# Kernel optimization log

Hardware: AMD Instinct MI355X
Metric: run time of the kernel (lower is better)

Reference implementation:

```python
import jax, jax.numpy as jnp
import numpy as np

N, E, D, DE, DH = 8000, 15000, 128, 16, 128
NUM_STEPS = 3


def setup_inputs() -> dict:
    key = jax.random.key(0)
    ks = jax.random.split(key, 10)
    s = lambda k, shape, scale: jax.random.normal(k, shape, jnp.float32) * scale
    return {
        "x": jax.random.normal(ks[0], (N, D), jnp.float32),
        "edge_attr": jax.random.normal(ks[1], (E, DE), jnp.float32),
        "W0": s(ks[2], (D, D), 0.08),   # lin0
        "b0": jnp.zeros((D,), jnp.float32),
        "W1": s(ks[3], (DE, DH), 0.2),  # edge net layer 1
        "b1": jnp.zeros((DH,), jnp.float32),
        "W2": s(ks[4], (DH, D * D), 0.02),  # edge net layer 2 -> D*D
        "b2": jnp.zeros((D * D,), jnp.float32),
        "root": s(ks[5], (D, D), 0.08),  # NNConv root weight
        "bias": jnp.zeros((D,), jnp.float32),  # NNConv bias
        "Wm": s(ks[6], (2 * D, D), 0.08),  # message_layer
        "bm": jnp.zeros((D,), jnp.float32),
        "edge_index": jax.random.randint(ks[7], (2, E), 0, N, jnp.int32),
    }


def reference(x, edge_attr, W0, b0, W1, b1, W2, b2, root, bias, Wm, bm, edge_index):
    n, d = x.shape
    src, dst = edge_index[0], edge_index[1]  # source_to_target flow (PyG default)
    # edge-conditioned weight matrices, identical across steps since edge_attr is fixed: [E, D, D]
    ew = (jax.nn.relu(edge_attr @ W1 + b1) @ W2 + b2).reshape(-1, d, d)
    init = x
    out = jax.nn.relu(x @ W0 + b0)
    for _ in range(NUM_STEPS):
        # gather source features, per-edge matvec, scatter-add to destinations
        msg = jnp.einsum('ed,edo->eo', out[src], ew)  # [E, D]
        agg = jax.ops.segment_sum(msg, dst, num_segments=n)  # [N, D]
        m = jax.nn.relu(agg + out @ root + bias)  # NNConv with root_weight + bias, then relu
        out = jnp.concatenate([m, out], axis=1) @ Wm + bm  # message_layer
    return out + init
```

## Files before the change

kernel.cpp:

```cpp
#include <hip/hip_runtime.h>

#define NE   15000
#define NVX  8000
#define EPAD 15040
#define NT_E 235

typedef __attribute__((ext_vector_type(8))) short short8;
typedef __attribute__((ext_vector_type(4))) float f32x4;

static __device__ __forceinline__ unsigned short f2b(float f){
  unsigned int u = __float_as_uint(f);
  u += 0x7fffu + ((u >> 16) & 1u);
  return (unsigned short)(u >> 16);
}

__global__ __launch_bounds__(256) void k_cvt(const float* __restrict__ in,
                                             unsigned short* __restrict__ out, int n){
  int i = (blockIdx.x * 256 + threadIdx.x) * 4;
  if (i >= n) return;
  float4 v = *(const float4*)(in + i);
  ushort4 o;
  o.x = f2b(v.x); o.y = f2b(v.y); o.z = f2b(v.z); o.w = f2b(v.w);
  *(ushort4*)(out + i) = o;
}

__global__ __launch_bounds__(256) void k_h1(const float* __restrict__ ea,
                                            const float* __restrict__ W1,
                                            const float* __restrict__ b1,
                                            float* __restrict__ h1T){
  __shared__ float sW1[16*128];
  __shared__ float sb1[128];
  int t = threadIdx.x;
  #pragma unroll
  for (int i = 0; i < 8; ++i) sW1[i*256 + t] = W1[i*256 + t];
  if (t < 128) sb1[t] = b1[t];
  __syncthreads();
  int e = blockIdx.x * 64 + (t & 63);
  int hg = t >> 6;
  bool valid = e < NE;
  int esafe = valid ? e : 0;
  float a[16];
  #pragma unroll
  for (int i = 0; i < 4; ++i){
    float4 v = *(const float4*)(ea + (size_t)esafe*16 + i*4);
    a[i*4+0]=v.x; a[i*4+1]=v.y; a[i*4+2]=v.z; a[i*4+3]=v.w;
  }
  for (int hh = 0; hh < 32; ++hh){
    int h = hg*32 + hh;
    float s = sb1[h];
    #pragma unroll
    for (int k = 0; k < 16; ++k) s = fmaf(a[k], sW1[k*128 + h], s);
    s = fmaxf(s, 0.f);
    h1T[(size_t)h*EPAD + e] = valid ? s : 0.f;
  }
}

__global__ __launch_bounds__(256) void k_wt(const float* __restrict__ W2,
                                            const float* __restrict__ b2,
                                            const float* __restrict__ W0,
                                            const float* __restrict__ root,
                                            const float* __restrict__ Wm,
                                            unsigned short* __restrict__ W2T,
                                            unsigned short* __restrict__ sWt){
  int b = blockIdx.x;
  const float* src;
  unsigned short* out;
  if (b < 128)      { src = W2 + (size_t)b*16384; out = W2T + (size_t)b*16384; }
  else if (b == 128){ src = b2;                   out = W2T + (size_t)128*16384; }
  else {
    int s = b - 129;
    out = sWt + (size_t)s*16384;
    src = (s==0) ? W0 : (s==1) ? root : (s==2) ? Wm : (Wm + 128*128);
  }
  int t = threadIdx.x;
  int o = t & 127, half = t >> 7;
  for (int it = 0; it < 8; ++it){
    int d0 = half*64 + it*8;
    unsigned int pk[4];
    #pragma unroll
    for (int j = 0; j < 4; ++j){
      float v0 = src[(size_t)(d0 + 2*j    )*128 + o];
      float v1 = src[(size_t)(d0 + 2*j + 1)*128 + o];
      pk[j] = (unsigned int)f2b(v0) | ((unsigned int)f2b(v1) << 16);
    }
    unsigned int off = (unsigned int)(o*256 + d0*2) ^ (((unsigned int)(o & 7)) << 4);
    *(uint4*)((char*)out + off) = make_uint4(pk[0], pk[1], pk[2], pk[3]);
  }
}

__global__ __launch_bounds__(256,2) void k_big(const unsigned short* __restrict__ outcur,
                                               const unsigned short* __restrict__ W2T,
                                               const float* __restrict__ h1T,
                                               const int* __restrict__ eidx,
                                               float* __restrict__ agg){
  __shared__ __align__(16) unsigned short sX[64*128];
  __shared__ __align__(16) float          sH[64*64];
  __shared__ __align__(16) unsigned short sW[128*128];
  int t = threadIdx.x, l = t & 63, w = t >> 6;
  int tile = blockIdx.x >> 1, par = blockIdx.x & 1;
  int e0 = tile * 64;
  {
    int r = t >> 2, q = t & 3;
    int e = e0 + r;
    int srow = eidx[e < NE ? e : NE-1];
    const uint4* gp = (const uint4*)((const char*)outcur + (size_t)srow*256 + q*64);
    uint4* lp = (uint4*)((char*)sX + r*256 + q*64);
    #pragma unroll
    for (int i = 0; i < 4; ++i) lp[i] = gp[i];
  }
  {
    int hh = t >> 2, q = t & 3;
    int h = par + hh*2;
    const uint4* gp = (const uint4*)((const char*)h1T + ((size_t)h*EPAD + e0)*4 + q*64);
    uint4* lp = (uint4*)((char*)sH + hh*256 + q*64);
    #pragma unroll
    for (int i = 0; i < 4; ++i) lp[i] = gp[i];
  }
  __syncthreads();
  short8 af[4][4];
  #pragma unroll
  for (int mf = 0; mf < 4; ++mf)
    #pragma unroll
    for (int kf = 0; kf < 4; ++kf)
      af[mf][kf] = *(const short8*)((const char*)sX + (mf*16 + (l & 15))*256 + kf*64 + ((l >> 4)*16));
  f32x4 acc[4][2];
  #pragma unroll
  for (int mf = 0; mf < 4; ++mf)
    #pragma unroll
    for (int nf = 0; nf < 2; ++nf)
      acc[mf][nf] = (f32x4){0.f,0.f,0.f,0.f};
  const f32x4 zf = (f32x4){0.f,0.f,0.f,0.f};
  int nh = (par == 0) ? 65 : 64;
  for (int hh = 0; hh < nh; ++hh){
    int h = (hh < 64) ? (par + hh*2) : 128;
    __syncthreads();
    {
      const uint4* gp = (const uint4*)((const char*)W2T + (size_t)h*32768);
      uint4* lp = (uint4*)sW;
      #pragma unroll
      for (int i = 0; i < 8; ++i) lp[i*256 + t] = gp[i*256 + t];
    }
    __syncthreads();
    f32x4 hv[4];
    if (hh < 64){
      #pragma unroll
      for (int mf = 0; mf < 4; ++mf)
        hv[mf] = *(const f32x4*)((const char*)sH + hh*256 + mf*64 + ((l >> 4)*16));
    } else {
      #pragma unroll
      for (int mf = 0; mf < 4; ++mf){
        int rb = e0 + mf*16 + ((l >> 4) << 2);
        #pragma unroll
        for (int j = 0; j < 4; ++j) hv[mf][j] = (rb + j < NE) ? 1.f : 0.f;
      }
    }
    #pragma unroll
    for (int nf = 0; nf < 2; ++nf){
      int col = w*32 + nf*16 + (l & 15);
      unsigned int swz = ((unsigned int)(col & 7)) << 4;
      f32x4 Y[4];
      #pragma unroll
      for (int kf = 0; kf < 4; ++kf){
        short8 bfr = *(const short8*)((const char*)sW +
                        (((unsigned int)(col*256 + kf*64 + ((l >> 4)*16))) ^ swz));
        #pragma unroll
        for (int mf = 0; mf < 4; ++mf)
          Y[mf] = __builtin_amdgcn_mfma_f32_16x16x32_bf16(af[mf][kf], bfr,
                    (kf == 0) ? zf : Y[mf], 0, 0, 0);
      }
      #pragma unroll
      for (int mf = 0; mf < 4; ++mf)
        #pragma unroll
        for (int j = 0; j < 4; ++j)
          acc[mf][nf][j] = fmaf(hv[mf][j], Y[mf][j], acc[mf][nf][j]);
    }
  }
  #pragma unroll
  for (int mf = 0; mf < 4; ++mf){
    #pragma unroll
    for (int j = 0; j < 4; ++j){
      int e = e0 + mf*16 + ((l >> 4) << 2) + j;
      int dst = (e < NE) ? eidx[NE + e] : 0;
      float* ap = agg + (size_t)dst*128;
      #pragma unroll
      for (int nf = 0; nf < 2; ++nf){
        int col = w*32 + nf*16 + (l & 15);
        atomicAdd(ap + col, acc[mf][nf][j]);
      }
    }
  }
}

__global__ __launch_bounds__(256,2) void k_gsm(const unsigned short* __restrict__ Aa,
                                               const unsigned short* __restrict__ Wa,
                                               const unsigned short* __restrict__ Ab,
                                               const unsigned short* __restrict__ Wb,
                                               const float* __restrict__ addin,
                                               const float* __restrict__ bias,
                                               int do_relu,
                                               unsigned short* __restrict__ outb,
                                               float* __restrict__ outf){
  __shared__ __align__(16) unsigned short sA[64*128];
  __shared__ __align__(16) unsigned short sW[128*128];
  int t = threadIdx.x, l = t & 63, w = t >> 6;
  int r0 = blockIdx.x * 64;
  f32x4 acc[4][2];
  #pragma unroll
  for (int mf = 0; mf < 4; ++mf)
    #pragma unroll
    for (int nf = 0; nf < 2; ++nf)
      acc[mf][nf] = (f32x4){0.f,0.f,0.f,0.f};
  const unsigned short* A = Aa;
  const unsigned short* W = Wa;
  for (int pass = 0; pass < 2; ++pass){
    if (pass == 1){
      if (Ab == nullptr) break;
      A = Ab; W = Wb;
      __syncthreads();
    }
    {
      const uint4* gp = (const uint4*)((const char*)A + (size_t)r0*256);
      uint4* lp = (uint4*)sA;
      #pragma unroll
      for (int i = 0; i < 4; ++i) lp[i*256 + t] = gp[i*256 + t];
      const uint4* gw = (const uint4*)W;
      uint4* lw = (uint4*)sW;
      #pragma unroll
      for (int i = 0; i < 8; ++i) lw[i*256 + t] = gw[i*256 + t];
    }
    __syncthreads();
    short8 af[4][4];
    #pragma unroll
    for (int mf = 0; mf < 4; ++mf)
      #pragma unroll
      for (int kf = 0; kf < 4; ++kf)
        af[mf][kf] = *(const short8*)((const char*)sA + (mf*16 + (l & 15))*256 + kf*64 + ((l >> 4)*16));
    #pragma unroll
    for (int nf = 0; nf < 2; ++nf){
      int col = w*32 + nf*16 + (l & 15);
      unsigned int swz = ((unsigned int)(col & 7)) << 4;
      #pragma unroll
      for (int kf = 0; kf < 4; ++kf){
        short8 bfr = *(const short8*)((const char*)sW +
                        (((unsigned int)(col*256 + kf*64 + ((l >> 4)*16))) ^ swz));
        #pragma unroll
        for (int mf = 0; mf < 4; ++mf)
          acc[mf][nf] = __builtin_amdgcn_mfma_f32_16x16x32_bf16(af[mf][kf], bfr, acc[mf][nf], 0, 0, 0);
      }
    }
  }
  #pragma unroll
  for (int mf = 0; mf < 4; ++mf){
    #pragma unroll
    for (int nf = 0; nf < 2; ++nf){
      #pragma unroll
      for (int j = 0; j < 4; ++j){
        int r = r0 + mf*16 + ((l >> 4) << 2) + j;
        int c = w*32 + nf*16 + (l & 15);
        float v = acc[mf][nf][j];
        if (addin) v += addin[(size_t)r*128 + c];
        v += bias[c];
        if (do_relu) v = fmaxf(v, 0.f);
        if (outb) outb[(size_t)r*128 + c] = f2b(v);
        if (outf) outf[(size_t)r*128 + c] = v;
      }
    }
  }
}

extern "C" void kernel_launch(void* const* d_in, const int* in_sizes, int n_in,
                              void* d_out, int out_size, void* d_ws, size_t ws_size,
                              hipStream_t stream){
  (void)in_sizes; (void)n_in; (void)out_size; (void)ws_size;
  const float* x    = (const float*)d_in[0];
  const float* ea   = (const float*)d_in[1];
  const float* W0   = (const float*)d_in[2];
  const float* b0   = (const float*)d_in[3];
  const float* W1   = (const float*)d_in[4];
  const float* b1   = (const float*)d_in[5];
  const float* W2   = (const float*)d_in[6];
  const float* b2   = (const float*)d_in[7];
  const float* root = (const float*)d_in[8];
  const float* bias = (const float*)d_in[9];
  const float* Wm   = (const float*)d_in[10];
  const float* bm   = (const float*)d_in[11];
  const int*   eidx = (const int*)d_in[12];

  char* p = (char*)d_ws;
  unsigned short* W2T = (unsigned short*)p; p += (size_t)129*32768;
  unsigned short* sWt = (unsigned short*)p; p += (size_t)4*32768;
  float*          h1T = (float*)p;          p += (size_t)128*EPAD*4;
  unsigned short* xb  = (unsigned short*)p; p += (size_t)NVX*128*2;
  unsigned short* oA  = (unsigned short*)p; p += (size_t)NVX*128*2;
  unsigned short* oB  = (unsigned short*)p; p += (size_t)NVX*128*2;
  unsigned short* mB  = (unsigned short*)p; p += (size_t)NVX*128*2;
  float*          agg = (float*)p;          p += (size_t)NVX*128*4;

  k_cvt<<<1000, 256, 0, stream>>>(x, xb, NVX*128);
  k_h1 <<<NT_E, 256, 0, stream>>>(ea, W1, b1, h1T);
  k_wt <<<133,  256, 0, stream>>>(W2, b2, W0, root, Wm, W2T, sWt);
  k_gsm<<<125, 256, 0, stream>>>(xb, sWt + 0*16384,
                                 (const unsigned short*)nullptr, (const unsigned short*)nullptr,
                                 (const float*)nullptr, b0, 1, oA, (float*)nullptr);
  unsigned short* cur = oA;
  unsigned short* nxt = oB;
  for (int s = 0; s < 3; ++s){
    hipMemsetAsync(agg, 0, (size_t)NVX*128*4, stream);
    k_big<<<2*NT_E, 256, 0, stream>>>(cur, W2T, h1T, eidx, agg);
    k_gsm<<<125, 256, 0, stream>>>(cur, sWt + 1*16384,
                                   (const unsigned short*)nullptr, (const unsigned short*)nullptr,
                                   agg, bias, 1, mB, (float*)nullptr);
    if (s < 2){
      k_gsm<<<125, 256, 0, stream>>>(mB, sWt + 2*16384, cur, sWt + 3*16384,
                                     (const float*)nullptr, bm, 0, nxt, (float*)nullptr);
    } else {
      k_gsm<<<125, 256, 0, stream>>>(mB, sWt + 2*16384, cur, sWt + 3*16384,
                                     x, bm, 0, (unsigned short*)nullptr, (float*)d_out);
    }
    unsigned short* tsw = cur; cur = nxt; nxt = tsw;
  }
}
```

Before: 359.2 us.

## Enlarge edge tile to 128, load W2 fragments straight from global, fuse agg clear

```diff
diff --git a/kernel.cpp b/kernel.cpp
--- a/kernel.cpp
+++ b/kernel.cpp
@@ -2,8 +2,8 @@
 
 #define NE   15000
 #define NVX  8000
-#define EPAD 15040
-#define NT_E 235
+#define EPAD 15104
+#define NT_E 118
 
 typedef __attribute__((ext_vector_type(8))) short short8;
 typedef __attribute__((ext_vector_type(4))) float f32x4;
@@ -88,105 +88,92 @@
   }
 }
 
-__global__ __launch_bounds__(256,2) void k_big(const unsigned short* __restrict__ outcur,
+__global__ __launch_bounds__(512,2) void k_big(const unsigned short* __restrict__ outcur,
                                                const unsigned short* __restrict__ W2T,
                                                const float* __restrict__ h1T,
                                                const int* __restrict__ eidx,
                                                float* __restrict__ agg){
-  __shared__ __align__(16) unsigned short sX[64*128];
-  __shared__ __align__(16) float          sH[64*64];
-  __shared__ __align__(16) unsigned short sW[128*128];
+  __shared__ __align__(16) unsigned short sX[128*128];
   int t = threadIdx.x, l = t & 63, w = t >> 6;
   int tile = blockIdx.x >> 1, par = blockIdx.x & 1;
-  int e0 = tile * 64;
+  int e0 = tile * 128;
   {
     int r = t >> 2, q = t & 3;
     int e = e0 + r;
     int srow = eidx[e < NE ? e : NE-1];
-    const uint4* gp = (const uint4*)((const char*)outcur + (size_t)srow*256 + q*64);
-    uint4* lp = (uint4*)((char*)sX + r*256 + q*64);
-    #pragma unroll
-    for (int i = 0; i < 4; ++i) lp[i] = gp[i];
-  }
-  {
-    int hh = t >> 2, q = t & 3;
-    int h = par + hh*2;
-    const uint4* gp = (const uint4*)((const char*)h1T + ((size_t)h*EPAD + e0)*4 + q*64);
-    uint4* lp = (uint4*)((char*)sH + hh*256 + q*64);
-    #pragma unroll
-    for (int i = 0; i < 4; ++i) lp[i] = gp[i];
+    const uint4* gp = (const uint4*)(outcur + (size_t)srow*128);
+    #pragma unroll
+    for (int i = 0; i < 4; ++i){
+      uint4 v = gp[q*4 + i];
+      unsigned off = (unsigned)((q*64 + i*16) ^ ((r & 7) << 4));
+      *(uint4*)((char*)sX + r*256 + off) = v;
+    }
   }
   __syncthreads();
-  short8 af[4][4];
-  #pragma unroll
-  for (int mf = 0; mf < 4; ++mf)
-    #pragma unroll
-    for (int kf = 0; kf < 4; ++kf)
-      af[mf][kf] = *(const short8*)((const char*)sX + (mf*16 + (l & 15))*256 + kf*64 + ((l >> 4)*16));
-  f32x4 acc[4][2];
-  #pragma unroll
-  for (int mf = 0; mf < 4; ++mf)
-    #pragma unroll
-    for (int nf = 0; nf < 2; ++nf)
-      acc[mf][nf] = (f32x4){0.f,0.f,0.f,0.f};
+  short8 af[8][4];
+  #pragma unroll
+  for (int mf = 0; mf < 8; ++mf){
+    int row = mf*16 + (l & 15);
+    #pragma unroll
+    for (int kf = 0; kf < 4; ++kf){
+      unsigned off = (unsigned)((kf*64 + ((l >> 4)*16)) ^ ((row & 7) << 4));
+      af[mf][kf] = *(const short8*)((const char*)sX + row*256 + off);
+    }
+  }
+  f32x4 acc[8];
+  #pragma unroll
+  for (int mf = 0; mf < 8; ++mf) acc[mf] = (f32x4){0.f,0.f,0.f,0.f};
+  int colc = w*16 + (l & 15);
+  unsigned offB[4];
+  #pragma unroll
+  for (int kf = 0; kf < 4; ++kf)
+    offB[kf] = (unsigned)((colc*256 + kf*64 + ((l >> 4)*16)) ^ ((colc & 7) << 4));
+  const float* hbase = h1T + e0 + ((l >> 4) << 2);
+  const char* wb2 = (const char*)W2T;
   const f32x4 zf = (f32x4){0.f,0.f,0.f,0.f};
-  int nh = (par == 0) ? 65 : 64;
+  int nh = 64 + ((par == 0) ? 1 : 0);
   for (int hh = 0; hh < nh; ++hh){
-    int h = (hh < 64) ? (par + hh*2) : 128;
-    __syncthreads();
-    {
-      const uint4* gp = (const uint4*)((const char*)W2T + (size_t)h*32768);
-      uint4* lp = (uint4*)sW;
-      #pragma unroll
-      for (int i = 0; i < 8; ++i) lp[i*256 + t] = gp[i*256 + t];
-    }
-    __syncthreads();
-    f32x4 hv[4];
-    if (hh < 64){
-      #pragma unroll
-      for (int mf = 0; mf < 4; ++mf)
-        hv[mf] = *(const f32x4*)((const char*)sH + hh*256 + mf*64 + ((l >> 4)*16));
-    } else {
-      #pragma unroll
-      for (int mf = 0; mf < 4; ++mf){
-        int rb = e0 + mf*16 + ((l >> 4) << 2);
-        #pragma unroll
-        for (int j = 0; j < 4; ++j) hv[mf][j] = (rb + j < NE) ? 1.f : 0.f;
+    int h = (hh < 64) ? (par + 2*hh) : 128;
+    const char* wb = wb2 + (size_t)h * 32768;
+    short8 bq[4];
+    #pragma unroll
+    for (int kf = 0; kf < 4; ++kf) bq[kf] = *(const short8*)(wb + offB[kf]);
+    const float* hp = hbase + (size_t)h * EPAD;
+    #pragma unroll
+    for (int half = 0; half < 2; ++half){
+      f32x4 Y[4];
+      #pragma unroll
+      for (int kf = 0; kf < 4; ++kf)
+        #pragma unroll
+        for (int m4 = 0; m4 < 4; ++m4)
+          Y[m4] = __builtin_amdgcn_mfma_f32_16x16x32_bf16(af[half*4+m4][kf], bq[kf],
+                    (kf == 0) ? zf : Y[m4], 0, 0, 0);
+      f32x4 hv[4];
+      if (hh < 64){
+        #pragma unroll
+        for (int m4 = 0; m4 < 4; ++m4) hv[m4] = *(const f32x4*)(hp + (half*4+m4)*16);
+      } else {
+        #pragma unroll
+        for (int m4 = 0; m4 < 4; ++m4){
+          int rb = e0 + (half*4+m4)*16 + ((l >> 4) << 2);
+          #pragma unroll
+          for (int j = 0; j < 4; ++j) hv[m4][j] = (rb + j < NE) ? 1.f : 0.f;
+        }
       }
-    }
-    #pragma unroll
-    for (int nf = 0; nf < 2; ++nf){
-      int col = w*32 + nf*16 + (l & 15);
-      unsigned int swz = ((unsigned int)(col & 7)) << 4;
-      f32x4 Y[4];
-      #pragma unroll
-      for (int kf = 0; kf < 4; ++kf){
-        short8 bfr = *(const short8*)((const char*)sW +
-                        (((unsigned int)(col*256 + kf*64 + ((l >> 4)*16))) ^ swz));
-        #pragma unroll
-        for (int mf = 0; mf < 4; ++mf)
-          Y[mf] = __builtin_amdgcn_mfma_f32_16x16x32_bf16(af[mf][kf], bfr,
-                    (kf == 0) ? zf : Y[mf], 0, 0, 0);
-      }
-      #pragma unroll
-      for (int mf = 0; mf < 4; ++mf)
+      #pragma unroll
+      for (int m4 = 0; m4 < 4; ++m4)
         #pragma unroll
         for (int j = 0; j < 4; ++j)
-          acc[mf][nf][j] = fmaf(hv[mf][j], Y[mf][j], acc[mf][nf][j]);
-    }
-  }
-  #pragma unroll
-  for (int mf = 0; mf < 4; ++mf){
+          acc[half*4+m4][j] = fmaf(hv[m4][j], Y[m4][j], acc[half*4+m4][j]);
+    }
+  }
+  #pragma unroll
+  for (int mf = 0; mf < 8; ++mf){
     #pragma unroll
     for (int j = 0; j < 4; ++j){
       int e = e0 + mf*16 + ((l >> 4) << 2) + j;
       int dst = (e < NE) ? eidx[NE + e] : 0;
-      float* ap = agg + (size_t)dst*128;
-      #pragma unroll
-      for (int nf = 0; nf < 2; ++nf){
-        int col = w*32 + nf*16 + (l & 15);
-        atomicAdd(ap + col, acc[mf][nf][j]);
-      }
+      atomicAdd(agg + (size_t)dst*128 + colc, acc[mf][j]);
     }
   }
 }
@@ -196,6 +183,7 @@
                                                const unsigned short* __restrict__ Ab,
                                                const unsigned short* __restrict__ Wb,
                                                const float* __restrict__ addin,
+                                               float* __restrict__ clr,
                                                const float* __restrict__ bias,
                                                int do_relu,
                                                unsigned short* __restrict__ outb,
@@ -259,6 +247,7 @@
         int c = w*32 + nf*16 + (l & 15);
         float v = acc[mf][nf][j];
         if (addin) v += addin[(size_t)r*128 + c];
+        if (clr)   clr[(size_t)r*128 + c] = 0.f;
         v += bias[c];
         if (do_relu) v = fmaxf(v, 0.f);
         if (outb) outb[(size_t)r*128 + c] = f2b(v);
@@ -297,25 +286,25 @@
   float*          agg = (float*)p;          p += (size_t)NVX*128*4;
 
   k_cvt<<<1000, 256, 0, stream>>>(x, xb, NVX*128);
-  k_h1 <<<NT_E, 256, 0, stream>>>(ea, W1, b1, h1T);
+  k_h1 <<<EPAD/64, 256, 0, stream>>>(ea, W1, b1, h1T);
   k_wt <<<133,  256, 0, stream>>>(W2, b2, W0, root, Wm, W2T, sWt);
   k_gsm<<<125, 256, 0, stream>>>(xb, sWt + 0*16384,
                                  (const unsigned short*)nullptr, (const unsigned short*)nullptr,
-                                 (const float*)nullptr, b0, 1, oA, (float*)nullptr);
+                                 (const float*)nullptr, (float*)nullptr, b0, 1, oA, (float*)nullptr);
   unsigned short* cur = oA;
   unsigned short* nxt = oB;
   for (int s = 0; s < 3; ++s){
-    hipMemsetAsync(agg, 0, (size_t)NVX*128*4, stream);
-    k_big<<<2*NT_E, 256, 0, stream>>>(cur, W2T, h1T, eidx, agg);
+    if (s == 0) hipMemsetAsync(agg, 0, (size_t)NVX*128*4, stream);
+    k_big<<<2*NT_E, 512, 0, stream>>>(cur, W2T, h1T, eidx, agg);
     k_gsm<<<125, 256, 0, stream>>>(cur, sWt + 1*16384,
                                    (const unsigned short*)nullptr, (const unsigned short*)nullptr,
-                                   agg, bias, 1, mB, (float*)nullptr);
+                                   agg, (s < 2) ? agg : (float*)nullptr, bias, 1, mB, (float*)nullptr);
     if (s < 2){
       k_gsm<<<125, 256, 0, stream>>>(mB, sWt + 2*16384, cur, sWt + 3*16384,
-                                     (const float*)nullptr, bm, 0, nxt, (float*)nullptr);
+                                     (const float*)nullptr, (float*)nullptr, bm, 0, nxt, (float*)nullptr);
     } else {
       k_gsm<<<125, 256, 0, stream>>>(mB, sWt + 2*16384, cur, sWt + 3*16384,
-                                     x, bm, 0, (unsigned short*)nullptr, (float*)d_out);
+                                     x, (float*)nullptr, bm, 0, (unsigned short*)nullptr, (float*)d_out);
     }
     unsigned short* tsw = cur; cur = nxt; nxt = tsw;
   }
```

After: 424.2 us. 1.18x slower.
